# Optimization experiments

Hardware: AMD Instinct MI355X
Metric: run time of the kernel (lower is better)

The kernel has to match this reference:

```python
import jax, jax.numpy as jnp
import numpy as np

E = 1_600_000      # num edges
N = 50_000         # num nodes
G = 100            # num graphs in batch
EMB = 128          # emb_size
OUT = 256          # out_emb_size
NRAD = 6           # num_radial
NDENSE = 3         # num_dense


def setup_inputs() -> dict:
    key = jax.random.key(0)
    ks = jax.random.split(key, 8)
    m = jax.random.normal(ks[0], (E, EMB), dtype=jnp.float32)
    rbf = jax.random.normal(ks[1], (E, NRAD), dtype=jnp.float32)
    src = jax.random.randint(ks[2], (E,), 0, N, dtype=jnp.int64)
    graph_ids = jnp.sort(jax.random.randint(ks[3], (N,), 0, G, dtype=jnp.int64))
    # parameters (torch Linear convention: W [out, in])
    W_rbf = jax.random.normal(ks[4], (EMB, NRAD), dtype=jnp.float32) / np.sqrt(NRAD)
    W_up = jax.random.normal(ks[5], (OUT, EMB), dtype=jnp.float32) / np.sqrt(EMB)
    W_dense = jax.random.normal(ks[6], (NDENSE, OUT, OUT), dtype=jnp.float32) / np.sqrt(OUT)
    b_dense = jnp.zeros((NDENSE, OUT), dtype=jnp.float32)
    return {"m": m, "rbf": rbf, "src": src, "graph_ids": graph_ids,
            "W_rbf": W_rbf, "W_up": W_up, "W_dense": W_dense, "b_dense": b_dense}


def reference(m, rbf, src, graph_ids, W_rbf, W_up, W_dense, b_dense):
    # edge transform: tmp = m * dense_rbf(rbf)            [E, EMB]
    tmp = m * jnp.einsum('er,fr->ef', rbf, W_rbf)
    # reverse-graph copy_e/sum == scatter-sum onto original src nodes
    t = jax.ops.segment_sum(tmp, src, num_segments=N)     # [N, EMB]
    # up projection (no bias)
    t = jnp.einsum('ne,oe->no', t, W_up)                  # [N, OUT]
    # dense MLP with SiLU
    for i in range(NDENSE):
        t = jax.nn.silu(jnp.einsum('no,po->np', t, W_dense[i]) + b_dense[i])
    # extensive readout: per-graph sum
    out = jax.ops.segment_sum(t, graph_ids, num_segments=G)  # [G, OUT]
    return out
```

## Files before the change

### kernel.cpp

```cpp
#include <hip/hip_runtime.h>
#include <hip/hip_bf16.h>

typedef __attribute__((ext_vector_type(8))) short short8;
typedef __attribute__((ext_vector_type(4))) float f32x4;

#define EMB 128
#define OUT 256
#define NRAD 6
#define NDENSE 3
#define BSH 7
#define MAXBKT 512
#define HB 256

static __device__ __forceinline__ unsigned short f32_to_bf16(float f) {
    union { float f; unsigned u; } v; v.f = f;
    unsigned r = v.u + 0x7fffu + ((v.u >> 16) & 1u);
    return (unsigned short)(r >> 16);
}
static __device__ __forceinline__ float bf16_to_f32(unsigned short h) {
    union { unsigned u; float f; } v; v.u = ((unsigned)h) << 16;
    return v.f;
}
static __device__ __forceinline__ float silu(float x) {
    return x / (1.f + __expf(-x));
}
static __device__ __forceinline__ void gload_lds16(const void* gp, void* lp) {
    __builtin_amdgcn_global_load_lds(
        (const __attribute__((address_space(1))) void*)gp,
        (__attribute__((address_space(3))) void*)lp, 16, 0, 0);
}

__global__ __launch_bounds__(256) void init_kernel(
        const float* __restrict__ Wup, const float* __restrict__ Wd,
        unsigned short* __restrict__ Wbf, float* __restrict__ out, int outn) {
    int i = blockIdx.x * blockDim.x + threadIdx.x;
    int stride = gridDim.x * blockDim.x;
    for (int j = i; j < outn; j += stride) out[j] = 0.f;
    const int n1 = OUT * EMB, n2 = NDENSE * OUT * OUT;
    for (int j = i; j < n1 + n2; j += stride)
        Wbf[j] = f32_to_bf16(j < n1 ? Wup[j] : Wd[j - n1]);
}

__global__ __launch_bounds__(256) void bhist_kernel(
        const int* __restrict__ src, int* __restrict__ bpart, int E, int nbkt) {
    __shared__ int h[MAXBKT];
    for (int b = threadIdx.x; b < nbkt; b += 256) h[b] = 0;
    __syncthreads();
    int stride = gridDim.x * blockDim.x;
    for (int e = blockIdx.x * blockDim.x + threadIdx.x; e < E; e += stride)
        atomicAdd(&h[src[e] >> BSH], 1);
    __syncthreads();
    int* row = bpart + (size_t)blockIdx.x * MAXBKT;
    for (int b = threadIdx.x; b < nbkt; b += 256) row[b] = h[b];
}

__global__ __launch_bounds__(512) void bscan_kernel(
        const int* __restrict__ bpart, int* __restrict__ bbase,
        int* __restrict__ gcursor, int nbkt, int E) {
    __shared__ int s[MAXBKT];
    int t = threadIdx.x;
    int v = 0;
    if (t < nbkt) {
#pragma unroll 8
        for (int k = 0; k < HB; ++k) v += bpart[(size_t)k * MAXBKT + t];
    }
    s[t] = v;
    __syncthreads();
    for (int d = 1; d < MAXBKT; d <<= 1) {
        int x = (t >= d) ? s[t - d] : 0;
        __syncthreads();
        s[t] += x;
        __syncthreads();
    }
    if (t < nbkt) {
        int ex = s[t] - v;
        bbase[t] = ex;
        gcursor[t] = ex;
    }
    if (t == 0) bbase[nbkt] = E;
}

__global__ __launch_bounds__(256) void bscatter_kernel(
        const int* __restrict__ src, int* __restrict__ gcursor,
        int2* __restrict__ pairs, int E, int nbkt) {
    __shared__ int h[MAXBKT];
    __shared__ int base[MAXBKT];
    for (int b = threadIdx.x; b < nbkt; b += 256) h[b] = 0;
    __syncthreads();
    const int per = (E + gridDim.x - 1) / gridDim.x;
    const int e0 = blockIdx.x * per;
    const int e1 = min(e0 + per, E);
    for (int e = e0 + threadIdx.x; e < e1; e += 256)
        atomicAdd(&h[src[e] >> BSH], 1);
    __syncthreads();
    for (int b = threadIdx.x; b < nbkt; b += 256)
        base[b] = h[b] ? atomicAdd(&gcursor[b], h[b]) : 0;
    __syncthreads();
    for (int e = e0 + threadIdx.x; e < e1; e += 256) {
        int s = src[e];
        int pos = atomicAdd(&base[s >> BSH], 1);
        pairs[pos] = make_int2(e, s);
    }
}

__global__ __launch_bounds__(256) void local_csr_kernel(
        const int2* __restrict__ pairs, const int* __restrict__ bbase,
        int* __restrict__ offsets, int* __restrict__ perm, int N, int E, int nbkt) {
    __shared__ int cnt[128], exc[128], cur[128];
    const int b = blockIdx.x;
    const int t = threadIdx.x;
    const int n0 = b << BSH;
    const int nn = min(128, N - n0);
    const int p0 = bbase[b], p1 = bbase[b + 1];
    if (t < 128) cnt[t] = 0;
    __syncthreads();
    for (int i = p0 + t; i < p1; i += 256)
        atomicAdd(&cnt[pairs[i].y - n0], 1);
    __syncthreads();
    if (t < 128) exc[t] = cnt[t];
    __syncthreads();
    for (int d = 1; d < 128; d <<= 1) {
        int x = (t >= d && t < 128) ? exc[t - d] : 0;
        __syncthreads();
        if (t < 128) exc[t] += x;
        __syncthreads();
    }
    if (t < 128) {
        int ex = exc[t] - cnt[t];
        cur[t] = ex;
        if (t < nn) offsets[n0 + t] = p0 + ex;
    }
    if (b == 0 && t == 0) offsets[N] = E;
    __syncthreads();
    for (int i = p0 + t; i < p1; i += 256) {
        int2 pr = pairs[i];
        int pos = p0 + atomicAdd(&cur[pr.y - n0], 1);
        perm[pos] = pr.x;
    }
}

__global__ __launch_bounds__(256) void edge_accum_kernel(
        const float* __restrict__ m, const float* __restrict__ rbf,
        const int* __restrict__ perm, const int* __restrict__ offsets,
        const float* __restrict__ W_rbf, uint2* __restrict__ t_pack, int N) {
    const int lane = threadIdx.x & 63;
    const int h = lane >> 5;
    const int c = lane & 31;
    const int gw = blockIdx.x * (blockDim.x >> 6) + (threadIdx.x >> 6);
    const int nwaves = gridDim.x * (blockDim.x >> 6);

    float wk[4][6];
#pragma unroll
    for (int k = 0; k < 4; ++k)
#pragma unroll
        for (int j = 0; j < 6; ++j) wk[k][j] = W_rbf[(4 * c + k) * NRAD + j];

    for (int node = gw; node < N; node += nwaves) {
        const int beg = offsets[node], end = offsets[node + 1];
        float a0 = 0.f, a1 = 0.f, a2 = 0.f, a3 = 0.f;
        int pe = 0;
        if (beg < end) {
            int pi = beg + (lane & 15); if (pi > end - 1) pi = end - 1;
            pe = perm[pi];
        }
        for (int cb = beg; cb < end; cb += 16) {
            int pe_next = 0;
            if (cb + 16 < end) {
                int pi = cb + 16 + (lane & 15); if (pi > end - 1) pi = end - 1;
                pe_next = perm[pi];
            }
#pragma unroll
            for (int p = 0; p < 8; ++p) {
                int e = __shfl(pe, 2 * p + h);
                const float2* rp = (const float2*)(rbf + (size_t)e * NRAD);
                float2 r0 = rp[0], r1 = rp[1], r2 = rp[2];
                float4 mv = *(const float4*)(m + (size_t)e * EMB + 4 * c);
                float g = (cb + 2 * p + h < end) ? 1.f : 0.f;
                float p0 = (wk[0][0]*r0.x + wk[0][1]*r0.y + wk[0][2]*r1.x
                          + wk[0][3]*r1.y + wk[0][4]*r2.x + wk[0][5]*r2.y) * g;
                float p1 = (wk[1][0]*r0.x + wk[1][1]*r0.y + wk[1][2]*r1.x
                          + wk[1][3]*r1.y + wk[1][4]*r2.x + wk[1][5]*r2.y) * g;
                float p2 = (wk[2][0]*r0.x + wk[2][1]*r0.y + wk[2][2]*r1.x
                          + wk[2][3]*r1.y + wk[2][4]*r2.x + wk[2][5]*r2.y) * g;
                float p3 = (wk[3][0]*r0.x + wk[3][1]*r0.y + wk[3][2]*r1.x
                          + wk[3][3]*r1.y + wk[3][4]*r2.x + wk[3][5]*r2.y) * g;
                a0 = fmaf(mv.x, p0, a0);
                a1 = fmaf(mv.y, p1, a1);
                a2 = fmaf(mv.z, p2, a2);
                a3 = fmaf(mv.w, p3, a3);
            }
            pe = pe_next;
        }
        a0 += __shfl_xor(a0, 32);
        a1 += __shfl_xor(a1, 32);
        a2 += __shfl_xor(a2, 32);
        a3 += __shfl_xor(a3, 32);
        if (h == 0) {
            uint2 pk;
            pk.x = (unsigned)f32_to_bf16(a0) | ((unsigned)f32_to_bf16(a1) << 16);
            pk.y = (unsigned)f32_to_bf16(a2) | ((unsigned)f32_to_bf16(a3) << 16);
            t_pack[(size_t)node * 32 + c] = pk;
        }
    }
}

__global__ __launch_bounds__(256) void fused_mlp2_kernel(
        const unsigned short* __restrict__ A0,
        const unsigned short* __restrict__ Wup,
        const unsigned short* __restrict__ Wd,
        const float* __restrict__ bd,
        unsigned short* __restrict__ Hout, int M) {
    __shared__ char Abuf[32768];
    __shared__ char Wbuf[32768];
    const int t    = threadIdx.x;
    const int w    = t >> 6;
    const int lane = t & 63;
    const int r    = lane & 15;
    const int g    = lane >> 4;
    const int row0 = blockIdx.x * 64;

    f32x4 acc[4][4];

#pragma unroll
    for (int it = 0; it < 4; ++it) {
        int unit = it * 256 + t;
        int row  = unit >> 4;
        int seg  = unit & 15;
        int csrc = (seg * 16) ^ ((row & 7) << 4);
        int ga = row0 + row; if (ga >= M) ga = M - 1;
        gload_lds16((const char*)A0 + (size_t)ga * 256 + csrc, Abuf + unit * 16);
    }

#pragma unroll
    for (int i = 0; i < 4; ++i)
#pragma unroll
        for (int j = 0; j < 4; ++j) acc[i][j] = (f32x4){0.f, 0.f, 0.f, 0.f};
#pragma unroll
    for (int kci = 0; kci < 2; ++kci) {
        const int kc = kci * 64;
        if (kci) __syncthreads();
#pragma unroll
        for (int it = 0; it < 8; ++it) {
            int unit = it * 256 + t;
            int wrow = unit >> 3;
            int seg  = unit & 7;
            int csrc = (seg * 16) ^ ((wrow & 7) << 4);
            gload_lds16((const char*)Wup + (size_t)wrow * 256 + kc * 2 + csrc,
                        Wbuf + unit * 16);
        }
        asm volatile("s_waitcnt vmcnt(0)" ::: "memory");
        __syncthreads();
#pragma unroll
        for (int ks = 0; ks < 2; ++ks) {
            short8 af[4], bf[4];
#pragma unroll
            for (int mi = 0; mi < 4; ++mi) {
                int row = mi * 16 + r;
                int off = kc * 2 + ks * 64 + g * 16;
                af[mi] = *(const short8*)(Abuf + row * 256 + (off ^ ((row & 7) << 4)));
            }
#pragma unroll
            for (int nj = 0; nj < 4; ++nj) {
                int col = w * 64 + nj * 16 + r;
                bf[nj] = *(const short8*)(Wbuf + col * 128
                          + ((ks * 64 + g * 16) ^ ((col & 7) << 4)));
            }
#pragma unroll
            for (int mi = 0; mi < 4; ++mi)
#pragma unroll
                for (int nj = 0; nj < 4; ++nj)
                    acc[mi][nj] = __builtin_amdgcn_mfma_f32_16x16x32_bf16(
                        af[mi], bf[nj], acc[mi][nj], 0, 0, 0);
        }
    }
    __syncthreads();
#pragma unroll
    for (int mi = 0; mi < 4; ++mi)
#pragma unroll
        for (int nj = 0; nj < 4; ++nj)
#pragma unroll
            for (int q = 0; q < 4; ++q) {
                int row = mi * 16 + g * 4 + q;
                int col = w * 64 + nj * 16 + r;
                *(unsigned short*)(Abuf + row * 512 + ((col * 2) ^ ((row & 7) << 4)))
                    = f32_to_bf16(acc[mi][nj][q]);
            }
    __syncthreads();

    for (int ell = 0; ell < NDENSE; ++ell) {
        const unsigned short* Wl = Wd + (size_t)ell * OUT * OUT;
        const float* bias = bd + ell * OUT;
#pragma unroll
        for (int i = 0; i < 4; ++i)
#pragma unroll
            for (int j = 0; j < 4; ++j) acc[i][j] = (f32x4){0.f, 0.f, 0.f, 0.f};
#pragma unroll
        for (int kci = 0; kci < 4; ++kci) {
            const int kc = kci * 64;
            __syncthreads();
#pragma unroll
            for (int it = 0; it < 8; ++it) {
                int unit = it * 256 + t;
                int wrow = unit >> 3;
                int seg  = unit & 7;
                int csrc = (seg * 16) ^ ((wrow & 7) << 4);
                gload_lds16((const char*)Wl + (size_t)wrow * 512 + kc * 2 + csrc,
                            Wbuf + unit * 16);
            }
            asm volatile("s_waitcnt vmcnt(0)" ::: "memory");
            __syncthreads();
#pragma unroll
            for (int ks = 0; ks < 2; ++ks) {
                short8 af[4], bf[4];
#pragma unroll
                for (int mi = 0; mi < 4; ++mi) {
                    int row = mi * 16 + r;
                    int off = kc * 2 + ks * 64 + g * 16;
                    af[mi] = *(const short8*)(Abuf + row * 512 + (off ^ ((row & 7) << 4)));
                }
#pragma unroll
                for (int nj = 0; nj < 4; ++nj) {
                    int col = w * 64 + nj * 16 + r;
                    bf[nj] = *(const short8*)(Wbuf + col * 128
                              + ((ks * 64 + g * 16) ^ ((col & 7) << 4)));
                }
#pragma unroll
                for (int mi = 0; mi < 4; ++mi)
#pragma unroll
                    for (int nj = 0; nj < 4; ++nj)
                        acc[mi][nj] = __builtin_amdgcn_mfma_f32_16x16x32_bf16(
                            af[mi], bf[nj], acc[mi][nj], 0, 0, 0);
            }
        }
        __syncthreads();
        if (ell < NDENSE - 1) {
#pragma unroll
            for (int mi = 0; mi < 4; ++mi)
#pragma unroll
                for (int nj = 0; nj < 4; ++nj) {
                    int col = w * 64 + nj * 16 + r;
                    float b = bias[col];
#pragma unroll
                    for (int q = 0; q < 4; ++q) {
                        int row = mi * 16 + g * 4 + q;
                        *(unsigned short*)(Abuf + row * 512
                            + ((col * 2) ^ ((row & 7) << 4)))
                            = f32_to_bf16(silu(acc[mi][nj][q] + b));
                    }
                }
            __syncthreads();
        } else {
#pragma unroll
            for (int nj = 0; nj < 4; ++nj) {
                int gcol = w * 64 + nj * 16 + r;
                float b = bias[gcol];
#pragma unroll
                for (int mi = 0; mi < 4; ++mi)
#pragma unroll
                    for (int q = 0; q < 4; ++q) {
                        int grow = row0 + mi * 16 + g * 4 + q;
                        if (grow < M)
                            Hout[(size_t)grow * OUT + gcol]
                                = f32_to_bf16(silu(acc[mi][nj][q] + b));
                    }
            }
        }
    }
}

__global__ __launch_bounds__(256) void graph_partial_kernel(
        const unsigned short* __restrict__ h, const int* __restrict__ gids,
        float* __restrict__ out, int M) {
    int gph = blockIdx.x, s = blockIdx.y;
    int c = threadIdx.x;
    int lo = 0, hi = M;
    while (lo < hi) { int mid = (lo + hi) >> 1; if (gids[mid] < gph) lo = mid + 1; else hi = mid; }
    int lo2 = lo, hi2 = M;
    while (lo2 < hi2) { int mid = (lo2 + hi2) >> 1; if (gids[mid] < gph + 1) lo2 = mid + 1; else hi2 = mid; }
    int len = lo2 - lo;
    int q = (len + 3) >> 2;
    int b0 = lo + s * q;
    int b1 = b0 + q; if (b1 > lo2) b1 = lo2;
    float a0 = 0.f, a1 = 0.f;
    int n = b0;
    for (; n + 1 < b1; n += 2) {
        a0 += bf16_to_f32(h[(size_t)n * OUT + c]);
        a1 += bf16_to_f32(h[(size_t)(n + 1) * OUT + c]);
    }
    for (; n < b1; ++n) a0 += bf16_to_f32(h[(size_t)n * OUT + c]);
    float v = a0 + a1;
    if (b0 < b1) atomicAdd(&out[(size_t)gph * OUT + c], v);
}

extern "C" void kernel_launch(void* const* d_in, const int* in_sizes, int n_in,
                              void* d_out, int out_size, void* d_ws, size_t ws_size,
                              hipStream_t stream) {
    const float* m         = (const float*)d_in[0];
    const float* rbf       = (const float*)d_in[1];
    const int*   src       = (const int*)d_in[2];
    const int*   gids      = (const int*)d_in[3];
    const float* W_rbf     = (const float*)d_in[4];
    const float* W_up      = (const float*)d_in[5];
    const float* W_dense   = (const float*)d_in[6];
    const float* b_dense   = (const float*)d_in[7];
    float* out = (float*)d_out;

    const int E = in_sizes[2];
    const int N = in_sizes[3];
    const int G = out_size / OUT;
    const int nbkt = (N + 127) >> BSH;

    size_t off = 0;
    auto alloc = [&](size_t bytes) -> void* {
        void* p = (char*)d_ws + off;
        off += (bytes + 255) & ~(size_t)255;
        return p;
    };
    int* bpart   = (int*)alloc((size_t)HB * MAXBKT * 4);
    int* bbase   = (int*)alloc((size_t)(MAXBKT + 1) * 4);
    int* gcursor = (int*)alloc((size_t)MAXBKT * 4);
    int* offsets = (int*)alloc(((size_t)N + 1) * 4);
    int2* pairs  = (int2*)alloc((size_t)E * 8);
    int* perm    = (int*)alloc((size_t)E * 4);
    unsigned short* t_bf = (unsigned short*)alloc((size_t)N * EMB * 2);
    unsigned short* h1   = (unsigned short*)alloc((size_t)N * OUT * 2);
    unsigned short* Wbf  = (unsigned short*)alloc((size_t)(OUT * EMB + NDENSE * OUT * OUT) * 2);
    unsigned short* Wup_bf = Wbf;
    unsigned short* Wd_bf  = Wbf + OUT * EMB;

    bhist_kernel<<<HB, 256, 0, stream>>>(src, bpart, E, nbkt);
    init_kernel<<<512, 256, 0, stream>>>(W_up, W_dense, Wbf, out, out_size);
    bscan_kernel<<<1, MAXBKT, 0, stream>>>(bpart, bbase, gcursor, nbkt, E);
    bscatter_kernel<<<512, 256, 0, stream>>>(src, gcursor, pairs, E, nbkt);
    local_csr_kernel<<<nbkt, 256, 0, stream>>>(pairs, bbase, offsets, perm, N, E, nbkt);

    edge_accum_kernel<<<2048, 256, 0, stream>>>(m, rbf, perm, offsets, W_rbf,
                                                (uint2*)t_bf, N);

    fused_mlp2_kernel<<<(N + 63) / 64, 256, 0, stream>>>(t_bf, Wup_bf, Wd_bf,
                                                         b_dense, h1, N);

    graph_partial_kernel<<<dim3(G, 4), 256, 0, stream>>>(h1, gids, out, N);
}
```

Baseline: 440.0 us.

## Fuse graph readout into MLP epilogue, merge init into histogram, widen edge batch

The per-graph segment sum now happens in the last MLP layer's epilogue. Tiles whose 64 rows all belong to one graph reduce in registers and shuffles before one atomic per column; mixed tiles fall back to per-element atomics. This removes the bf16 hidden-state buffer, its write and re-read, and the separate readout kernel. Weight conversion and output zeroing are folded into the histogram kernel to save a launch, and the edge-accumulation loop now processes 32 edges per batch instead of 16, which may raise register use. Readout sums are now in fp32 rather than bf16, and the atomic order is nondeterministic.

```diff
diff --git a/kernel.cpp b/kernel.cpp
--- a/kernel.cpp
+++ b/kernel.cpp
@@ -17,10 +17,6 @@
     unsigned r = v.u + 0x7fffu + ((v.u >> 16) & 1u);
     return (unsigned short)(r >> 16);
 }
-static __device__ __forceinline__ float bf16_to_f32(unsigned short h) {
-    union { unsigned u; float f; } v; v.u = ((unsigned)h) << 16;
-    return v.f;
-}
 static __device__ __forceinline__ float silu(float x) {
     return x / (1.f + __expf(-x));
 }
@@ -30,25 +26,22 @@
         (__attribute__((address_space(3))) void*)lp, 16, 0, 0);
 }
 
-__global__ __launch_bounds__(256) void init_kernel(
+__global__ __launch_bounds__(256) void setup_hist_kernel(
+        const int* __restrict__ src, int* __restrict__ bpart,
         const float* __restrict__ Wup, const float* __restrict__ Wd,
-        unsigned short* __restrict__ Wbf, float* __restrict__ out, int outn) {
-    int i = blockIdx.x * blockDim.x + threadIdx.x;
-    int stride = gridDim.x * blockDim.x;
-    for (int j = i; j < outn; j += stride) out[j] = 0.f;
-    const int n1 = OUT * EMB, n2 = NDENSE * OUT * OUT;
-    for (int j = i; j < n1 + n2; j += stride)
-        Wbf[j] = f32_to_bf16(j < n1 ? Wup[j] : Wd[j - n1]);
-}
-
-__global__ __launch_bounds__(256) void bhist_kernel(
-        const int* __restrict__ src, int* __restrict__ bpart, int E, int nbkt) {
+        unsigned short* __restrict__ Wbf, float* __restrict__ out,
+        int E, int nbkt, int outn) {
     __shared__ int h[MAXBKT];
     for (int b = threadIdx.x; b < nbkt; b += 256) h[b] = 0;
     __syncthreads();
+    int gtid = blockIdx.x * blockDim.x + threadIdx.x;
     int stride = gridDim.x * blockDim.x;
-    for (int e = blockIdx.x * blockDim.x + threadIdx.x; e < E; e += stride)
+    for (int e = gtid; e < E; e += stride)
         atomicAdd(&h[src[e] >> BSH], 1);
+    for (int j = gtid; j < outn; j += stride) out[j] = 0.f;
+    const int n1 = OUT * EMB, n2 = NDENSE * OUT * OUT;
+    for (int j = gtid; j < n1 + n2; j += stride)
+        Wbf[j] = f32_to_bf16(j < n1 ? Wup[j] : Wd[j - n1]);
     __syncthreads();
     int* row = bpart + (size_t)blockIdx.x * MAXBKT;
     for (int b = threadIdx.x; b < nbkt; b += 256) row[b] = h[b];
@@ -160,17 +153,17 @@
         float a0 = 0.f, a1 = 0.f, a2 = 0.f, a3 = 0.f;
         int pe = 0;
         if (beg < end) {
-            int pi = beg + (lane & 15); if (pi > end - 1) pi = end - 1;
+            int pi = beg + (lane & 31); if (pi > end - 1) pi = end - 1;
             pe = perm[pi];
         }
-        for (int cb = beg; cb < end; cb += 16) {
+        for (int cb = beg; cb < end; cb += 32) {
             int pe_next = 0;
-            if (cb + 16 < end) {
-                int pi = cb + 16 + (lane & 15); if (pi > end - 1) pi = end - 1;
+            if (cb + 32 < end) {
+                int pi = cb + 32 + (lane & 31); if (pi > end - 1) pi = end - 1;
                 pe_next = perm[pi];
             }
 #pragma unroll
-            for (int p = 0; p < 8; ++p) {
+            for (int p = 0; p < 16; ++p) {
                 int e = __shfl(pe, 2 * p + h);
                 const float2* rp = (const float2*)(rbf + (size_t)e * NRAD);
                 float2 r0 = rp[0], r1 = rp[1], r2 = rp[2];
@@ -209,7 +202,8 @@
         const unsigned short* __restrict__ Wup,
         const unsigned short* __restrict__ Wd,
         const float* __restrict__ bd,
-        unsigned short* __restrict__ Hout, int M) {
+        const int* __restrict__ gids,
+        float* __restrict__ out, int M) {
     __shared__ char Abuf[32768];
     __shared__ char Wbuf[32768];
     const int t    = threadIdx.x;
@@ -350,46 +344,42 @@
                 }
             __syncthreads();
         } else {
-#pragma unroll
-            for (int nj = 0; nj < 4; ++nj) {
-                int gcol = w * 64 + nj * 16 + r;
-                float b = bias[gcol];
-#pragma unroll
-                for (int mi = 0; mi < 4; ++mi)
-#pragma unroll
-                    for (int q = 0; q < 4; ++q) {
-                        int grow = row0 + mi * 16 + g * 4 + q;
-                        if (grow < M)
-                            Hout[(size_t)grow * OUT + gcol]
-                                = f32_to_bf16(silu(acc[mi][nj][q] + b));
-                    }
-            }
-        }
-    }
-}
-
-__global__ __launch_bounds__(256) void graph_partial_kernel(
-        const unsigned short* __restrict__ h, const int* __restrict__ gids,
-        float* __restrict__ out, int M) {
-    int gph = blockIdx.x, s = blockIdx.y;
-    int c = threadIdx.x;
-    int lo = 0, hi = M;
-    while (lo < hi) { int mid = (lo + hi) >> 1; if (gids[mid] < gph) lo = mid + 1; else hi = mid; }
-    int lo2 = lo, hi2 = M;
-    while (lo2 < hi2) { int mid = (lo2 + hi2) >> 1; if (gids[mid] < gph + 1) lo2 = mid + 1; else hi2 = mid; }
-    int len = lo2 - lo;
-    int q = (len + 3) >> 2;
-    int b0 = lo + s * q;
-    int b1 = b0 + q; if (b1 > lo2) b1 = lo2;
-    float a0 = 0.f, a1 = 0.f;
-    int n = b0;
-    for (; n + 1 < b1; n += 2) {
-        a0 += bf16_to_f32(h[(size_t)n * OUT + c]);
-        a1 += bf16_to_f32(h[(size_t)(n + 1) * OUT + c]);
-    }
-    for (; n < b1; ++n) a0 += bf16_to_f32(h[(size_t)n * OUT + c]);
-    float v = a0 + a1;
-    if (b0 < b1) atomicAdd(&out[(size_t)gph * OUT + c], v);
+            bool uni = (row0 + 63 < M) && (gids[row0] == gids[row0 + 63]);
+            if (uni) {
+                int gph = gids[row0];
+                float* og = out + (size_t)gph * OUT;
+#pragma unroll
+                for (int nj = 0; nj < 4; ++nj) {
+                    int gcol = w * 64 + nj * 16 + r;
+                    float b = bias[gcol];
+                    float s = 0.f;
+#pragma unroll
+                    for (int mi = 0; mi < 4; ++mi)
+#pragma unroll
+                        for (int q = 0; q < 4; ++q)
+                            s += silu(acc[mi][nj][q] + b);
+                    s += __shfl_xor(s, 16);
+                    s += __shfl_xor(s, 32);
+                    if (g == 0) atomicAdd(&og[gcol], s);
+                }
+            } else {
+#pragma unroll
+                for (int nj = 0; nj < 4; ++nj) {
+                    int gcol = w * 64 + nj * 16 + r;
+                    float b = bias[gcol];
+#pragma unroll
+                    for (int mi = 0; mi < 4; ++mi)
+#pragma unroll
+                        for (int q = 0; q < 4; ++q) {
+                            int grow = row0 + mi * 16 + g * 4 + q;
+                            if (grow < M)
+                                atomicAdd(&out[(size_t)gids[grow] * OUT + gcol],
+                                          silu(acc[mi][nj][q] + b));
+                        }
+                }
+            }
+        }
+    }
 }
 
 extern "C" void kernel_launch(void* const* d_in, const int* in_sizes, int n_in,
@@ -407,7 +397,6 @@
 
     const int E = in_sizes[2];
     const int N = in_sizes[3];
-    const int G = out_size / OUT;
     const int nbkt = (N + 127) >> BSH;
 
     size_t off = 0;
@@ -423,13 +412,12 @@
     int2* pairs  = (int2*)alloc((size_t)E * 8);
     int* perm    = (int*)alloc((size_t)E * 4);
     unsigned short* t_bf = (unsigned short*)alloc((size_t)N * EMB * 2);
-    unsigned short* h1   = (unsigned short*)alloc((size_t)N * OUT * 2);
     unsigned short* Wbf  = (unsigned short*)alloc((size_t)(OUT * EMB + NDENSE * OUT * OUT) * 2);
     unsigned short* Wup_bf = Wbf;
     unsigned short* Wd_bf  = Wbf + OUT * EMB;
 
-    bhist_kernel<<<HB, 256, 0, stream>>>(src, bpart, E, nbkt);
-    init_kernel<<<512, 256, 0, stream>>>(W_up, W_dense, Wbf, out, out_size);
+    setup_hist_kernel<<<HB, 256, 0, stream>>>(src, bpart, W_up, W_dense, Wbf,
+                                              out, E, nbkt, out_size);
     bscan_kernel<<<1, MAXBKT, 0, stream>>>(bpart, bbase, gcursor, nbkt, E);
     bscatter_kernel<<<512, 256, 0, stream>>>(src, gcursor, pairs, E, nbkt);
     local_csr_kernel<<<nbkt, 256, 0, stream>>>(pairs, bbase, offsets, perm, N, E, nbkt);
@@ -438,7 +426,5 @@
                                                 (uint2*)t_bf, N);
 
     fused_mlp2_kernel<<<(N + 63) / 64, 256, 0, stream>>>(t_bf, Wup_bf, Wd_bf,
-                                                         b_dense, h1, N);
-
-    graph_partial_kernel<<<dim3(G, 4), 256, 0, stream>>>(h1, gids, out, N);
-}
+                                                         b_dense, gids, out, N);
+}
```

New measurement: 423.1 us. -3.8%, faster.
